# Performance work log

Measured on AMD Instinct MI355X. Metric: run time of the kernel, lower is better.

## Reference

```python
import jax, jax.numpy as jnp
import numpy as np

B, L, E = 8, 2048, 128


def setup_inputs() -> dict:
    key = jax.random.key(0)
    k1, k2, k3, k4 = jax.random.split(key, 4)
    return {
        "Uq": jax.random.normal(k1, (B, L, E), dtype=jnp.float32),
        "Uid": jax.random.normal(k2, (B, L, E), dtype=jnp.float32),
        "mask": jnp.ones((L, L), dtype=jnp.float32),
        "Wc_w": jax.random.normal(k3, (3 * E,), dtype=jnp.float32) * 0.05,
        "Wc_b": jax.random.normal(k4, (), dtype=jnp.float32) * 0.05,
    }


def reference(Uq, Uid, mask, Wc_w, Wc_b):
    # Wc(cat(Uid, Uq, Uid*Uq)) decomposed into three direct projections —
    # exact same math as the Linear over the concatenation, never
    # materializing the [B, L, L, 3E] tensor.
    e = Uq.shape[-1]
    w_id, w_q, w_mul = Wc_w[:e], Wc_w[e:2 * e], Wc_w[2 * e:]
    s_id = jnp.einsum("bie,e->bi", Uid, w_id)          # [B, Lid]
    s_q = jnp.einsum("bje,e->bj", Uq, w_q)             # [B, Lq]
    s_mul = jnp.einsum("bie,bje,e->bij", Uid, Uq, w_mul)  # [B, Lid, Lq]
    S = (s_id[:, :, None] + s_q[:, None, :] + s_mul + Wc_b) * mask
    # S_D2Q = Softmax(dim=0) over the per-example [Lid, Lq] matrix -> axis=1
    P = jax.nn.softmax(S, axis=1)                      # [B, Lid, Lq]
    A_D2Q = jnp.einsum("bij,bje->bie", P, Uq)          # [B, Lid, E]
    M = jnp.einsum("bij,bkj->bik", P, P)               # P @ P^T, [B, Lid, Lid]
    A_Q2D = jnp.einsum("bik,bke->bie", M, Uid)         # [B, Lid, E]
    Vid = jnp.concatenate([Uid, A_D2Q, Uid * A_D2Q, Uid * A_Q2D], axis=-1)
    return Vid  # [B, Lid, 4E]
```

## Files before the change

kernel.cpp:

```cpp
#include <hip/hip_runtime.h>

#define L 2048
#define E 128
#define NB 8

typedef float f32x4 __attribute__((ext_vector_type(4)));
typedef short short8 __attribute__((ext_vector_type(8)));
typedef unsigned int u32;

static __device__ inline float bf2f(ushort u) {
  union { float f; u32 i; } v; v.i = ((u32)u) << 16; return v.f;
}
static __device__ inline ushort f2bf(float f) {
  union { float f; u32 i; } v; v.f = f;
  u32 x = v.i;
  return (ushort)((x + 0x7fffu + ((x >> 16) & 1u)) >> 16);
}

__device__ inline void glds16(const ushort* g, ushort* l) {
  __builtin_amdgcn_global_load_lds(
      (const __attribute__((address_space(1))) u32*)(const void*)g,
      (__attribute__((address_space(3))) u32*)(void*)l, 16, 0, 0);
}

__global__ __launch_bounds__(128) void k_prep(const float* __restrict__ Uq,
                                              const float* __restrict__ Uid,
                                              const float* __restrict__ Wcw,
                                              ushort* __restrict__ UqB,
                                              ushort* __restrict__ UidB,
                                              ushort* __restrict__ Uidw,
                                              float* __restrict__ s_id,
                                              float* __restrict__ s_q) {
  int r = blockIdx.x;
  int e = threadIdx.x;
  ushort uqu  = f2bf(Uq[(long)r * E + e]);
  ushort uidu = f2bf(Uid[(long)r * E + e]);
  float uqf = bf2f(uqu), uidf = bf2f(uidu);
  float wid  = bf2f(f2bf(Wcw[e]));
  float wq   = bf2f(f2bf(Wcw[E + e]));
  float wmul = bf2f(f2bf(Wcw[2 * E + e]));
  UqB[(long)r * E + e]  = uqu;
  UidB[(long)r * E + e] = uidu;
  Uidw[(long)r * E + e] = f2bf(uidf * wmul);
  float sid = uidf * wid, sq = uqf * wq;
  #pragma unroll
  for (int off = 32; off >= 1; off >>= 1) {
    sid += __shfl_down(sid, off, 64);
    sq  += __shfl_down(sq,  off, 64);
  }
  __shared__ float red[4];
  int wv = threadIdx.x >> 6;
  if ((threadIdx.x & 63) == 0) { red[wv * 2] = sid; red[wv * 2 + 1] = sq; }
  __syncthreads();
  if (threadIdx.x == 0) { s_id[r] = red[0] + red[2]; s_q[r] = red[1] + red[3]; }
}

__global__ __launch_bounds__(256) void k_maskT(const float* __restrict__ mask,
                                               ushort* __restrict__ maskT) {
  __shared__ ushort tile[32][33];
  int j0 = blockIdx.x * 32, i0 = blockIdx.y * 32;
  int tx = threadIdx.x, ty = threadIdx.y;
  #pragma unroll
  for (int r = ty; r < 32; r += 8)
    tile[r][tx] = f2bf(mask[(long)(i0 + r) * L + j0 + tx]);
  __syncthreads();
  #pragma unroll
  for (int r = ty; r < 32; r += 8)
    maskT[(long)(j0 + r) * L + i0 + tx] = tile[tx][r];
}

__global__ __launch_bounds__(256) void k_tr2(const ushort* __restrict__ s1,
                                             ushort* __restrict__ d1,
                                             const ushort* __restrict__ s2,
                                             ushort* __restrict__ d2) {
  __shared__ ushort tile[32][33];
  int zz = blockIdx.z;
  long base = (long)(zz & (NB - 1)) * L * E;
  const ushort* src = ((zz < NB) ? s1 : s2) + base;
  ushort* dst = ((zz < NB) ? d1 : d2) + base;
  int c0 = blockIdx.x * 32, r0 = blockIdx.y * 32;
  int tx = threadIdx.x, ty = threadIdx.y;
  #pragma unroll
  for (int i = ty; i < 32; i += 8)
    tile[i][tx] = src[(long)(r0 + i) * E + c0 + tx];
  __syncthreads();
  #pragma unroll
  for (int i = ty; i < 32; i += 8)
    dst[(long)(c0 + i) * L + r0 + tx] = tile[tx][i];
}

__device__ inline void gemm128_loop(const ushort* __restrict__ A,
                                    const ushort* __restrict__ B,
                                    long ldA, long ldB, int K,
                                    f32x4 acc[4][4],
                                    ushort* ldsA, ushort* ldsB) {
  const int t = threadIdx.x;
  const int w = t >> 6, lane = t & 63;
  const int mrow = lane & 15, quad = lane >> 4;
  const int lr = lane >> 3;
  const int lc = ((lane & 7) ^ lr) * 8;
  const int mh = (w & 1) * 64, nh = (w >> 1) * 64;
  for (int k0 = 0; k0 < K; k0 += 64) {
    __syncthreads();
    #pragma unroll
    for (int s = 0; s < 4; s++) {
      int row = w * 32 + s * 8 + lr;
      glds16(&A[(long)row * ldA + k0 + lc], &ldsA[w * 2048 + s * 512]);
      glds16(&B[(long)row * ldB + k0 + lc], &ldsB[w * 2048 + s * 512]);
    }
    __syncthreads();
    #pragma unroll
    for (int kk = 0; kk < 2; kk++) {
      short8 av[4], bv[4];
      #pragma unroll
      for (int mi = 0; mi < 4; mi++)
        av[mi] = *(const short8*)&ldsA[(mh + mi * 16 + mrow) * 64 +
                                       ((kk * 32 + quad * 8) ^ ((mrow & 7) << 3))];
      #pragma unroll
      for (int ni = 0; ni < 4; ni++)
        bv[ni] = *(const short8*)&ldsB[(nh + ni * 16 + mrow) * 64 +
                                       ((kk * 32 + quad * 8) ^ ((mrow & 7) << 3))];
      #pragma unroll
      for (int mi = 0; mi < 4; mi++)
        #pragma unroll
        for (int ni = 0; ni < 4; ni++)
          acc[mi][ni] = __builtin_amdgcn_mfma_f32_16x16x32_bf16(av[mi], bv[ni], acc[mi][ni], 0, 0, 0);
    }
  }
}

__device__ inline void gemm64x128_dbuf(const ushort* __restrict__ A,
                                       const ushort* __restrict__ B,
                                       long ldA, long ldB, int K,
                                       f32x4 acc[2][4],
                                       ushort* ldsA, ushort* ldsB) {
  const int t = threadIdx.x;
  const int w = t >> 6, lane = t & 63;
  const int mrow = lane & 15, quad = lane >> 4;
  const int lr = lane >> 3;
  const int lc = ((lane & 7) ^ lr) * 8;
  const int mh = (w & 1) * 32, nh = (w >> 1) * 64;
  #pragma unroll
  for (int s = 0; s < 2; s++) {
    int row = w * 16 + s * 8 + lr;
    glds16(&A[(long)row * ldA + lc], &ldsA[w * 1024 + s * 512]);
  }
  #pragma unroll
  for (int s = 0; s < 4; s++) {
    int row = w * 32 + s * 8 + lr;
    glds16(&B[(long)row * ldB + lc], &ldsB[w * 2048 + s * 512]);
  }
  int cur = 0;
  for (int k0 = 0; k0 < K; k0 += 64) {
    __syncthreads();
    int nxt = cur ^ 1;
    if (k0 + 64 < K) {
      #pragma unroll
      for (int s = 0; s < 2; s++) {
        int row = w * 16 + s * 8 + lr;
        glds16(&A[(long)row * ldA + k0 + 64 + lc], &ldsA[nxt * 4096 + w * 1024 + s * 512]);
      }
      #pragma unroll
      for (int s = 0; s < 4; s++) {
        int row = w * 32 + s * 8 + lr;
        glds16(&B[(long)row * ldB + k0 + 64 + lc], &ldsB[nxt * 8192 + w * 2048 + s * 512]);
      }
    }
    const ushort* cA = &ldsA[cur * 4096];
    const ushort* cB = &ldsB[cur * 8192];
    #pragma unroll
    for (int kk = 0; kk < 2; kk++) {
      short8 av[2], bv[4];
      #pragma unroll
      for (int mi = 0; mi < 2; mi++)
        av[mi] = *(const short8*)&cA[(mh + mi * 16 + mrow) * 64 +
                                     ((kk * 32 + quad * 8) ^ ((mrow & 7) << 3))];
      #pragma unroll
      for (int ni = 0; ni < 4; ni++)
        bv[ni] = *(const short8*)&cB[(nh + ni * 16 + mrow) * 64 +
                                     ((kk * 32 + quad * 8) ^ ((mrow & 7) << 3))];
      #pragma unroll
      for (int mi = 0; mi < 2; mi++)
        #pragma unroll
        for (int ni = 0; ni < 4; ni++)
          acc[mi][ni] = __builtin_amdgcn_mfma_f32_16x16x32_bf16(av[mi], bv[ni], acc[mi][ni], 0, 0, 0);
    }
    cur = nxt;
  }
}

__global__ __launch_bounds__(256) void k_scores(const ushort* __restrict__ Uq,
                                                const ushort* __restrict__ Uidw,
                                                const float* __restrict__ s_id,
                                                const float* __restrict__ s_q,
                                                const float* __restrict__ Wcb,
                                                const ushort* __restrict__ maskT,
                                                ushort* __restrict__ St,
                                                float* __restrict__ ps, int b0) {
  __shared__ ushort lds[16384];
  ushort* ldsA = lds;
  ushort* ldsB = lds + 8192;
  int bz = blockIdx.z, b = b0 + bz;
  int m0 = blockIdx.x * 128;
  int n0 = blockIdx.y * 128;
  int tile_i = blockIdx.y;
  const ushort* A = Uq   + (long)b * L * E + (long)m0 * E;
  const ushort* B = Uidw + (long)b * L * E + (long)n0 * E;
  f32x4 acc[4][4] = {};
  gemm128_loop(A, B, E, E, E, acc, ldsA, ldsB);
  float bias = bf2f(f2bf(Wcb[0]));
  const int t = threadIdx.x, w = t >> 6, lane = t & 63;
  const int col = lane & 15, quad = lane >> 4;
  const int mh = (w & 1) * 64, nh = (w >> 1) * 64;

  __syncthreads();
  float sidv[4];
  #pragma unroll
  for (int ni = 0; ni < 4; ni++)
    sidv[ni] = s_id[b * L + n0 + nh + ni * 16 + col];
  #pragma unroll
  for (int mi = 0; mi < 4; mi++) {
    float sqv[4];
    #pragma unroll
    for (int rg = 0; rg < 4; rg++)
      sqv[rg] = s_q[b * L + m0 + mh + mi * 16 + quad * 4 + rg];
    #pragma unroll
    for (int ni = 0; ni < 4; ni++) {
      int cl = nh + ni * 16 + col;
      #pragma unroll
      for (int rg = 0; rg < 4; rg++) {
        int row = mh + mi * 16 + quad * 4 + rg;
        float v = acc[mi][ni][rg] + sqv[rg] + sidv[ni] + bias;
        lds[row * 128 + (cl ^ ((row & 7) << 3))] = f2bf(v);
      }
    }
  }
  __syncthreads();
  #pragma unroll
  for (int p = 0; p < 8; p++) {
    int r2 = p * 16 + (t >> 4);
    int cu = (t & 15) * 8;
    uint4 sv = *(const uint4*)&lds[r2 * 128 + (cu ^ ((r2 & 7) << 3))];
    int jg = m0 + r2;
    uint4 mv = *(const uint4*)&maskT[(long)jg * L + n0 + cu];
    ushort o[8];
    float lsum = 0.f;
    const ushort* sp = (const ushort*)&sv;
    const ushort* mp = (const ushort*)&mv;
    #pragma unroll
    for (int k = 0; k < 8; k++) {
      float ev = __expf(bf2f(sp[k]) * bf2f(mp[k]));
      o[k] = f2bf(ev);
      lsum += bf2f(o[k]);
    }
    *(uint4*)&St[(long)bz * L * L + (long)jg * L + n0 + cu] = *(const uint4*)&o[0];
    #pragma unroll
    for (int off = 8; off >= 1; off >>= 1) lsum += __shfl_xor(lsum, off, 64);
    if ((t & 15) == 0) {
      ps[((long)bz * L + jg) * 16 + tile_i] = lsum;
    }
  }
}

__global__ __launch_bounds__(256) void k_redstats(const float* __restrict__ ps,
                                                  float* __restrict__ lg) {
  int idx = blockIdx.x * 256 + threadIdx.x;
  const float* psr = ps + (long)idx * 16;
  float s = 0.f;
  #pragma unroll
  for (int k = 0; k < 16; k++) s += psr[k];
  lg[idx] = 1.0f / s;
}

__global__ __launch_bounds__(256) void k_gemm_Tt(const ushort* __restrict__ UidT,
                                                 const ushort* __restrict__ Et,
                                                 const float* __restrict__ lg,
                                                 ushort* __restrict__ Tt, int b0) {
  __shared__ ushort lds[24576];
  ushort* ldsA = lds;
  ushort* ldsB = lds + 8192;
  int bz = blockIdx.z, b = b0 + bz;
  int e0 = (blockIdx.x & 1) * 64;
  int j0 = (blockIdx.x >> 1) * 128;
  const ushort* A = UidT + (long)b * E * L + (long)e0 * L;
  const ushort* B = Et   + (long)bz * L * L + (long)j0 * L;
  f32x4 acc[2][4] = {};
  gemm64x128_dbuf(A, B, L, L, L, acc, ldsA, ldsB);
  const int t = threadIdx.x, w = t >> 6, lane = t & 63;
  const int col = lane & 15, quad = lane >> 4;
  const int mh = (w & 1) * 32, nh = (w >> 1) * 64;
  __syncthreads();
  #pragma unroll
  for (int mi = 0; mi < 2; mi++)
    #pragma unroll
    for (int ni = 0; ni < 4; ni++) {
      int cl = nh + ni * 16 + col;
      float sc = lg[(long)bz * L + j0 + cl];
      #pragma unroll
      for (int rg = 0; rg < 4; rg++) {
        int row = mh + mi * 16 + quad * 4 + rg;
        lds[row * 128 + (cl ^ ((row & 7) << 3))] = f2bf(acc[mi][ni][rg] * sc);
      }
    }
  __syncthreads();
  #pragma unroll
  for (int p = 0; p < 4; p++) {
    int r2 = p * 16 + (t >> 4);
    int cu = (t & 15) * 8;
    uint4 v = *(const uint4*)&lds[r2 * 128 + (cu ^ ((r2 & 7) << 3))];
    *(uint4*)&Tt[(long)b * E * L + (long)(e0 + r2) * L + j0 + cu] = v;
  }
}

__global__ __launch_bounds__(256) void k_gemm_A(const ushort* __restrict__ Et,
                                                const ushort* __restrict__ UqT,
                                                const ushort* __restrict__ Tt,
                                                const ushort* __restrict__ UidB,
                                                const float* __restrict__ lg,
                                                float* __restrict__ out, int b0) {
  __shared__ ushort ldsA[2 * 4608];
  __shared__ ushort ldsB[2 * 8192];
  int bz = blockIdx.z, b = b0 + bz;
  int m0 = blockIdx.x * 64;
  int n0 = blockIdx.y * 128;
  const ushort* Eb = Et + (long)bz * L * L + m0;
  const float* lgb = lg + (long)bz * L;
  const ushort* B = (blockIdx.y == 0) ? (UqT + (long)b * E * L)
                                      : (Tt  + (long)b * E * L);
  const int t = threadIdx.x, w = t >> 6, lane = t & 63;
  const int mrow = lane & 15, quad = lane >> 4;
  const int lr = lane >> 3;
  const int lc = ((lane & 7) ^ lr) * 8;
  const int mh = (w & 1) * 32, nh = (w >> 1) * 64;
  const int jp2 = (t >> 3) * 2;
  const int ic  = (t & 7) * 8;
  f32x4 acc[2][4] = {};
  uint4 q0 = *(const uint4*)&Eb[(long)jp2 * L + ic];
  uint4 q1 = *(const uint4*)&Eb[(long)(jp2 + 1) * L + ic];
  float s0 = lgb[jp2], s1 = lgb[jp2 + 1];
  #pragma unroll
  for (int s = 0; s < 4; s++) {
    int row = w * 32 + s * 8 + lr;
    glds16(&B[(long)row * L + lc], &ldsB[w * 2048 + s * 512]);
  }
  {
    const ushort* p0 = (const ushort*)&q0;
    const ushort* p1 = (const ushort*)&q1;
    #pragma unroll
    for (int k = 0; k < 8; k++) {
      u32 pk = (u32)f2bf(bf2f(p0[k]) * s0) |
               ((u32)f2bf(bf2f(p1[k]) * s1) << 16);
      int i = ic + k;
      int cs = jp2 ^ (((i >> 3) & 7) << 3);
      *(u32*)&ldsA[i * 72 + cs] = pk;
    }
  }
  q0 = *(const uint4*)&Eb[(long)(64 + jp2) * L + ic];
  q1 = *(const uint4*)&Eb[(long)(64 + jp2 + 1) * L + ic];
  s0 = lgb[64 + jp2]; s1 = lgb[64 + jp2 + 1];

  int cur = 0;
  for (int k0 = 0; k0 < L; k0 += 64) {
    __syncthreads();
    int nxt = cur ^ 1;
    if (k0 + 64 < L) {
      #pragma unroll
      for (int s = 0; s < 4; s++) {
        int row = w * 32 + s * 8 + lr;
        glds16(&B[(long)row * L + k0 + 64 + lc], &ldsB[nxt * 8192 + w * 2048 + s * 512]);
      }
      const ushort* p0 = (const ushort*)&q0;
      const ushort* p1 = (const ushort*)&q1;
      #pragma unroll
      for (int k = 0; k < 8; k++) {
        u32 pk = (u32)f2bf(bf2f(p0[k]) * s0) |
                 ((u32)f2bf(bf2f(p1[k]) * s1) << 16);
        int i = ic + k;
        int cs = jp2 ^ (((i >> 3) & 7) << 3);
        *(u32*)&ldsA[nxt * 4608 + i * 72 + cs] = pk;
      }
    }
    if (k0 + 128 < L) {
      q0 = *(const uint4*)&Eb[(long)(k0 + 128 + jp2) * L + ic];
      q1 = *(const uint4*)&Eb[(long)(k0 + 128 + jp2 + 1) * L + ic];
      s0 = lgb[k0 + 128 + jp2]; s1 = lgb[k0 + 128 + jp2 + 1];
    }
    const ushort* cA = &ldsA[cur * 4608];
    const ushort* cB = &ldsB[cur * 8192];
    #pragma unroll
    for (int kk = 0; kk < 2; kk++) {
      short8 av[2], bv[4];
      #pragma unroll
      for (int mi = 0; mi < 2; mi++) {
        int i = mh + mi * 16 + mrow;
        av[mi] = *(const short8*)&cA[i * 72 +
                   ((kk * 32 + quad * 8) ^ (((i >> 3) & 7) << 3))];
      }
      #pragma unroll
      for (int ni = 0; ni < 4; ni++)
        bv[ni] = *(const short8*)&cB[(nh + ni * 16 + mrow) * 64 +
                                     ((kk * 32 + quad * 8) ^ ((mrow & 7) << 3))];
      #pragma unroll
      for (int mi = 0; mi < 2; mi++)
        #pragma unroll
        for (int ni = 0; ni < 4; ni++)
          acc[mi][ni] = __builtin_amdgcn_mfma_f32_16x16x32_bf16(av[mi], bv[ni], acc[mi][ni], 0, 0, 0);
    }
    cur = nxt;
  }
  const int col = mrow;
  #pragma unroll
  for (int mi = 0; mi < 2; mi++)
    #pragma unroll
    for (int ni = 0; ni < 4; ni++)
      #pragma unroll
      for (int rg = 0; rg < 4; rg++) {
        int ig = m0 + mh + mi * 16 + quad * 4 + rg;
        int c  = n0 + nh + ni * 16 + col;
        float a = acc[mi][ni][rg];
        float uidf = bf2f(UidB[(long)b * L * E + (long)ig * E + (c & 127)]);
        long ob = ((long)b * L + ig) * 512;
        if (c < 128) {
          out[ob + c]       = uidf;
          out[ob + 128 + c] = a;
          out[ob + 256 + c] = uidf * a;
        } else {
          out[ob + 256 + c] = uidf * a;
        }
      }
}

extern "C" void kernel_launch(void* const* d_in, const int* in_sizes, int n_in,
                              void* d_out, int out_size, void* d_ws, size_t ws_size,
                              hipStream_t stream) {
  const float* Uq   = (const float*)d_in[0];
  const float* Uid  = (const float*)d_in[1];
  const float* mask = (const float*)d_in[2];
  const float* Wcw  = (const float*)d_in[3];
  const float* Wcb  = (const float*)d_in[4];
  float* out = (float*)d_out;

  char* ws = (char*)d_ws;
  size_t off = 0;
  auto alloc = [&](size_t bytes) -> void* {
    void* p = ws + off; off += (bytes + 255) & ~(size_t)255; return p;
  };
  const size_t nUb = (size_t)NB * L * E * 2;
  ushort* UqB   = (ushort*)alloc(nUb);
  ushort* UidB  = (ushort*)alloc(nUb);
  ushort* Uidw  = (ushort*)alloc(nUb);
  ushort* UqT   = (ushort*)alloc(nUb);
  ushort* UidT  = (ushort*)alloc(nUb);
  ushort* Tt    = (ushort*)alloc(nUb);
  ushort* maskT = (ushort*)alloc((size_t)L * L * 2);
  float*  s_id  = (float*)alloc((size_t)NB * L * 4);
  float*  s_q   = (float*)alloc((size_t)NB * L * 4);
  float*  lg    = (float*)alloc((size_t)NB * L * 4);
  float*  ps    = (float*)alloc((size_t)NB * L * 16 * 4);
  const size_t per_batch = (size_t)L * L * 2;
  size_t avail = (ws_size > off + per_batch) ? (ws_size - off) : per_batch;
  int nb_c = (int)(avail / per_batch);
  if (nb_c < 1) nb_c = 1;
  if (nb_c > NB) nb_c = NB;
  ushort* St = (ushort*)(ws + off);

  dim3 tb(32, 8);
  k_prep<<<NB * L, E, 0, stream>>>(Uq, Uid, Wcw, UqB, UidB, Uidw, s_id, s_q);
  k_maskT<<<dim3(L / 32, L / 32), tb, 0, stream>>>(mask, maskT);
  k_tr2<<<dim3(E / 32, L / 32, 2 * NB), tb, 0, stream>>>(UqB, UqT, UidB, UidT);

  for (int b0 = 0; b0 < NB; b0 += nb_c) {
    int nb = (NB - b0 < nb_c) ? (NB - b0) : nb_c;
    k_scores<<<dim3(L / 128, L / 128, nb), 256, 0, stream>>>(UqB, Uidw, s_id, s_q, Wcb, maskT, St, ps, b0);
    k_redstats<<<dim3(nb * L / 256), 256, 0, stream>>>(ps, lg);
    k_gemm_Tt<<<dim3(2 * (L / 128), 1, nb), 256, 0, stream>>>(UidT, St, lg, Tt, b0);
    k_gemm_A<<<dim3(L / 64, 2, nb), 256, 0, stream>>>(St, UqT, Tt, UidB, lg, out, b0);
  }
}
```

Measured before the change: 205.7 us.

## Shrink Tt GEMM tiles, widen gemm_A to 8 waves, defer score stores

k_gemm_Tt now uses a 64x64 output tile instead of 64x128, which doubles the block count and shrinks its LDS footprint. k_gemm_A runs 512 threads (8 waves), so each wave owns a 32x32 sub-tile and stages half as much E data per iteration. k_scores buffers all eight exp'd rows in registers and writes St only after the row-sum reductions, separating global stores from the shuffle work. The aim is more parallelism and latency hiding in the GEMM stages. The cost is lower per-wave MFMA reuse, more register pressure in k_scores, and more redundant A-tile loads in the Tt GEMM.

```diff
diff --git a/kernel.cpp b/kernel.cpp
--- a/kernel.cpp
+++ b/kernel.cpp
@@ -129,26 +129,22 @@
   }
 }
 
-__device__ inline void gemm64x128_dbuf(const ushort* __restrict__ A,
-                                       const ushort* __restrict__ B,
-                                       long ldA, long ldB, int K,
-                                       f32x4 acc[2][4],
-                                       ushort* ldsA, ushort* ldsB) {
+__device__ inline void gemm64x64_dbuf(const ushort* __restrict__ A,
+                                      const ushort* __restrict__ B,
+                                      long ldA, long ldB, int K,
+                                      f32x4 acc[2][2],
+                                      ushort* ldsA, ushort* ldsB) {
   const int t = threadIdx.x;
   const int w = t >> 6, lane = t & 63;
   const int mrow = lane & 15, quad = lane >> 4;
   const int lr = lane >> 3;
   const int lc = ((lane & 7) ^ lr) * 8;
-  const int mh = (w & 1) * 32, nh = (w >> 1) * 64;
+  const int mh = (w & 1) * 32, nh = (w >> 1) * 32;
   #pragma unroll
   for (int s = 0; s < 2; s++) {
     int row = w * 16 + s * 8 + lr;
     glds16(&A[(long)row * ldA + lc], &ldsA[w * 1024 + s * 512]);
-  }
-  #pragma unroll
-  for (int s = 0; s < 4; s++) {
-    int row = w * 32 + s * 8 + lr;
-    glds16(&B[(long)row * ldB + lc], &ldsB[w * 2048 + s * 512]);
+    glds16(&B[(long)row * ldB + lc], &ldsB[w * 1024 + s * 512]);
   }
   int cur = 0;
   for (int k0 = 0; k0 < K; k0 += 64) {
@@ -159,30 +155,26 @@
       for (int s = 0; s < 2; s++) {
         int row = w * 16 + s * 8 + lr;
         glds16(&A[(long)row * ldA + k0 + 64 + lc], &ldsA[nxt * 4096 + w * 1024 + s * 512]);
-      }
-      #pragma unroll
-      for (int s = 0; s < 4; s++) {
-        int row = w * 32 + s * 8 + lr;
-        glds16(&B[(long)row * ldB + k0 + 64 + lc], &ldsB[nxt * 8192 + w * 2048 + s * 512]);
+        glds16(&B[(long)row * ldB + k0 + 64 + lc], &ldsB[nxt * 4096 + w * 1024 + s * 512]);
       }
     }
     const ushort* cA = &ldsA[cur * 4096];
-    const ushort* cB = &ldsB[cur * 8192];
+    const ushort* cB = &ldsB[cur * 4096];
     #pragma unroll
     for (int kk = 0; kk < 2; kk++) {
-      short8 av[2], bv[4];
+      short8 av[2], bv[2];
       #pragma unroll
       for (int mi = 0; mi < 2; mi++)
         av[mi] = *(const short8*)&cA[(mh + mi * 16 + mrow) * 64 +
                                      ((kk * 32 + quad * 8) ^ ((mrow & 7) << 3))];
       #pragma unroll
-      for (int ni = 0; ni < 4; ni++)
+      for (int ni = 0; ni < 2; ni++)
         bv[ni] = *(const short8*)&cB[(nh + ni * 16 + mrow) * 64 +
                                      ((kk * 32 + quad * 8) ^ ((mrow & 7) << 3))];
       #pragma unroll
       for (int mi = 0; mi < 2; mi++)
         #pragma unroll
-        for (int ni = 0; ni < 4; ni++)
+        for (int ni = 0; ni < 2; ni++)
           acc[mi][ni] = __builtin_amdgcn_mfma_f32_16x16x32_bf16(av[mi], bv[ni], acc[mi][ni], 0, 0, 0);
     }
     cur = nxt;
@@ -236,6 +228,7 @@
     }
   }
   __syncthreads();
+  ushort oall[64];
   #pragma unroll
   for (int p = 0; p < 8; p++) {
     int r2 = p * 16 + (t >> 4);
@@ -243,22 +236,27 @@
     uint4 sv = *(const uint4*)&lds[r2 * 128 + (cu ^ ((r2 & 7) << 3))];
     int jg = m0 + r2;
     uint4 mv = *(const uint4*)&maskT[(long)jg * L + n0 + cu];
-    ushort o[8];
     float lsum = 0.f;
     const ushort* sp = (const ushort*)&sv;
     const ushort* mp = (const ushort*)&mv;
     #pragma unroll
     for (int k = 0; k < 8; k++) {
       float ev = __expf(bf2f(sp[k]) * bf2f(mp[k]));
-      o[k] = f2bf(ev);
-      lsum += bf2f(o[k]);
-    }
-    *(uint4*)&St[(long)bz * L * L + (long)jg * L + n0 + cu] = *(const uint4*)&o[0];
+      oall[p * 8 + k] = f2bf(ev);
+      lsum += bf2f(oall[p * 8 + k]);
+    }
     #pragma unroll
     for (int off = 8; off >= 1; off >>= 1) lsum += __shfl_xor(lsum, off, 64);
     if ((t & 15) == 0) {
       ps[((long)bz * L + jg) * 16 + tile_i] = lsum;
     }
+  }
+  #pragma unroll
+  for (int p = 0; p < 8; p++) {
+    int r2 = p * 16 + (t >> 4);
+    int cu = (t & 15) * 8;
+    int jg = m0 + r2;
+    *(uint4*)&St[(long)bz * L * L + (long)jg * L + n0 + cu] = *(const uint4*)&oall[p * 8];
   }
 }
 
@@ -276,43 +274,43 @@
                                                  const ushort* __restrict__ Et,
                                                  const float* __restrict__ lg,
                                                  ushort* __restrict__ Tt, int b0) {
-  __shared__ ushort lds[24576];
+  __shared__ ushort lds[16384];
   ushort* ldsA = lds;
   ushort* ldsB = lds + 8192;
   int bz = blockIdx.z, b = b0 + bz;
   int e0 = (blockIdx.x & 1) * 64;
-  int j0 = (blockIdx.x >> 1) * 128;
+  int j0 = (blockIdx.x >> 1) * 64;
   const ushort* A = UidT + (long)b * E * L + (long)e0 * L;
   const ushort* B = Et   + (long)bz * L * L + (long)j0 * L;
-  f32x4 acc[2][4] = {};
-  gemm64x128_dbuf(A, B, L, L, L, acc, ldsA, ldsB);
+  f32x4 acc[2][2] = {};
+  gemm64x64_dbuf(A, B, L, L, L, acc, ldsA, ldsB);
   const int t = threadIdx.x, w = t >> 6, lane = t & 63;
   const int col = lane & 15, quad = lane >> 4;
-  const int mh = (w & 1) * 32, nh = (w >> 1) * 64;
+  const int mh = (w & 1) * 32, nh = (w >> 1) * 32;
   __syncthreads();
   #pragma unroll
   for (int mi = 0; mi < 2; mi++)
     #pragma unroll
-    for (int ni = 0; ni < 4; ni++) {
+    for (int ni = 0; ni < 2; ni++) {
       int cl = nh + ni * 16 + col;
       float sc = lg[(long)bz * L + j0 + cl];
       #pragma unroll
       for (int rg = 0; rg < 4; rg++) {
         int row = mh + mi * 16 + quad * 4 + rg;
-        lds[row * 128 + (cl ^ ((row & 7) << 3))] = f2bf(acc[mi][ni][rg] * sc);
-      }
-    }
-  __syncthreads();
-  #pragma unroll
-  for (int p = 0; p < 4; p++) {
-    int r2 = p * 16 + (t >> 4);
-    int cu = (t & 15) * 8;
-    uint4 v = *(const uint4*)&lds[r2 * 128 + (cu ^ ((r2 & 7) << 3))];
+        lds[row * 64 + (cl ^ ((row & 7) << 3))] = f2bf(acc[mi][ni][rg] * sc);
+      }
+    }
+  __syncthreads();
+  #pragma unroll
+  for (int p = 0; p < 2; p++) {
+    int r2 = p * 32 + (t >> 3);
+    int cu = (t & 7) * 8;
+    uint4 v = *(const uint4*)&lds[r2 * 64 + (cu ^ ((r2 & 7) << 3))];
     *(uint4*)&Tt[(long)b * E * L + (long)(e0 + r2) * L + j0 + cu] = v;
   }
 }
 
-__global__ __launch_bounds__(256) void k_gemm_A(const ushort* __restrict__ Et,
+__global__ __launch_bounds__(512) void k_gemm_A(const ushort* __restrict__ Et,
                                                 const ushort* __restrict__ UqT,
                                                 const ushort* __restrict__ Tt,
                                                 const ushort* __restrict__ UidB,
@@ -331,23 +329,23 @@
   const int mrow = lane & 15, quad = lane >> 4;
   const int lr = lane >> 3;
   const int lc = ((lane & 7) ^ lr) * 8;
-  const int mh = (w & 1) * 32, nh = (w >> 1) * 64;
-  const int jp2 = (t >> 3) * 2;
-  const int ic  = (t & 7) * 8;
-  f32x4 acc[2][4] = {};
-  uint4 q0 = *(const uint4*)&Eb[(long)jp2 * L + ic];
-  uint4 q1 = *(const uint4*)&Eb[(long)(jp2 + 1) * L + ic];
+  const int mh = (w & 1) * 32, nh = (w >> 1) * 32;
+  const int jp2 = (t >> 4) * 2;
+  const int ic  = (t & 15) * 4;
+  f32x4 acc[2][2] = {};
+  uint2 q0 = *(const uint2*)&Eb[(long)jp2 * L + ic];
+  uint2 q1 = *(const uint2*)&Eb[(long)(jp2 + 1) * L + ic];
   float s0 = lgb[jp2], s1 = lgb[jp2 + 1];
   #pragma unroll
-  for (int s = 0; s < 4; s++) {
-    int row = w * 32 + s * 8 + lr;
-    glds16(&B[(long)row * L + lc], &ldsB[w * 2048 + s * 512]);
+  for (int s = 0; s < 2; s++) {
+    int row = w * 16 + s * 8 + lr;
+    glds16(&B[(long)row * L + lc], &ldsB[w * 1024 + s * 512]);
   }
   {
     const ushort* p0 = (const ushort*)&q0;
     const ushort* p1 = (const ushort*)&q1;
     #pragma unroll
-    for (int k = 0; k < 8; k++) {
+    for (int k = 0; k < 4; k++) {
       u32 pk = (u32)f2bf(bf2f(p0[k]) * s0) |
                ((u32)f2bf(bf2f(p1[k]) * s1) << 16);
       int i = ic + k;
@@ -355,8 +353,8 @@
       *(u32*)&ldsA[i * 72 + cs] = pk;
     }
   }
-  q0 = *(const uint4*)&Eb[(long)(64 + jp2) * L + ic];
-  q1 = *(const uint4*)&Eb[(long)(64 + jp2 + 1) * L + ic];
+  q0 = *(const uint2*)&Eb[(long)(64 + jp2) * L + ic];
+  q1 = *(const uint2*)&Eb[(long)(64 + jp2 + 1) * L + ic];
   s0 = lgb[64 + jp2]; s1 = lgb[64 + jp2 + 1];
 
   int cur = 0;
@@ -365,14 +363,14 @@
     int nxt = cur ^ 1;
     if (k0 + 64 < L) {
       #pragma unroll
-      for (int s = 0; s < 4; s++) {
-        int row = w * 32 + s * 8 + lr;
-        glds16(&B[(long)row * L + k0 + 64 + lc], &ldsB[nxt * 8192 + w * 2048 + s * 512]);
+      for (int s = 0; s < 2; s++) {
+        int row = w * 16 + s * 8 + lr;
+        glds16(&B[(long)row * L + k0 + 64 + lc], &ldsB[nxt * 8192 + w * 1024 + s * 512]);
       }
       const ushort* p0 = (const ushort*)&q0;
       const ushort* p1 = (const ushort*)&q1;
       #pragma unroll
-      for (int k = 0; k < 8; k++) {
+      for (int k = 0; k < 4; k++) {
         u32 pk = (u32)f2bf(bf2f(p0[k]) * s0) |
                  ((u32)f2bf(bf2f(p1[k]) * s1) << 16);
         int i = ic + k;
@@ -381,15 +379,15 @@
       }
     }
     if (k0 + 128 < L) {
-      q0 = *(const uint4*)&Eb[(long)(k0 + 128 + jp2) * L + ic];
-      q1 = *(const uint4*)&Eb[(long)(k0 + 128 + jp2 + 1) * L + ic];
+      q0 = *(const uint2*)&Eb[(long)(k0 + 128 + jp2) * L + ic];
+      q1 = *(const uint2*)&Eb[(long)(k0 + 128 + jp2 + 1) * L + ic];
       s0 = lgb[k0 + 128 + jp2]; s1 = lgb[k0 + 128 + jp2 + 1];
     }
     const ushort* cA = &ldsA[cur * 4608];
     const ushort* cB = &ldsB[cur * 8192];
     #pragma unroll
     for (int kk = 0; kk < 2; kk++) {
-      short8 av[2], bv[4];
+      short8 av[2], bv[2];
       #pragma unroll
       for (int mi = 0; mi < 2; mi++) {
         int i = mh + mi * 16 + mrow;
@@ -397,13 +395,13 @@
                    ((kk * 32 + quad * 8) ^ (((i >> 3) & 7) << 3))];
       }
       #pragma unroll
-      for (int ni = 0; ni < 4; ni++)
+      for (int ni = 0; ni < 2; ni++)
         bv[ni] = *(const short8*)&cB[(nh + ni * 16 + mrow) * 64 +
                                      ((kk * 32 + quad * 8) ^ ((mrow & 7) << 3))];
       #pragma unroll
       for (int mi = 0; mi < 2; mi++)
         #pragma unroll
-        for (int ni = 0; ni < 4; ni++)
+        for (int ni = 0; ni < 2; ni++)
           acc[mi][ni] = __builtin_amdgcn_mfma_f32_16x16x32_bf16(av[mi], bv[ni], acc[mi][ni], 0, 0, 0);
     }
     cur = nxt;
@@ -412,7 +410,7 @@
   #pragma unroll
   for (int mi = 0; mi < 2; mi++)
     #pragma unroll
-    for (int ni = 0; ni < 4; ni++)
+    for (int ni = 0; ni < 2; ni++)
       #pragma unroll
       for (int rg = 0; rg < 4; rg++) {
         int ig = m0 + mh + mi * 16 + quad * 4 + rg;
@@ -473,7 +471,7 @@
     int nb = (NB - b0 < nb_c) ? (NB - b0) : nb_c;
     k_scores<<<dim3(L / 128, L / 128, nb), 256, 0, stream>>>(UqB, Uidw, s_id, s_q, Wcb, maskT, St, ps, b0);
     k_redstats<<<dim3(nb * L / 256), 256, 0, stream>>>(ps, lg);
-    k_gemm_Tt<<<dim3(2 * (L / 128), 1, nb), 256, 0, stream>>>(UidT, St, lg, Tt, b0);
-    k_gemm_A<<<dim3(L / 64, 2, nb), 256, 0, stream>>>(St, UqT, Tt, UidB, lg, out, b0);
-  }
-}
+    k_gemm_Tt<<<dim3(2 * (L / 64), 1, nb), 256, 0, stream>>>(UidT, St, lg, Tt, b0);
+    k_gemm_A<<<dim3(L / 64, 2, nb), 512, 0, stream>>>(St, UqT, Tt, UidB, lg, out, b0);
+  }
+}
```

New measurement: 203.9 us. No clear change (-0.8%).
